# Kernel optimization log

Hardware: AMD Instinct MI355X
Metric: run time of the kernel (lower is better)

## Reference

```python
import jax, jax.numpy as jnp
from jax import lax
import numpy as np

B = 16384
EPS = 1e-5


def conv2d(x, w, b, pad):
    # x: [N,C,H,W], w: [O,I,kh,kw]
    y = lax.conv_general_dilated(x, w, (1, 1), [(pad, pad), (pad, pad)],
                                 dimension_numbers=("NCHW", "OIHW", "NCHW"))
    return y + b[None, :, None, None]


def maxpool2(x):
    return lax.reduce_window(x, -jnp.inf, lax.max, (1, 1, 2, 2), (1, 1, 2, 2), "VALID")


def setup_inputs() -> dict:
    key = jax.random.key(0)
    ks = jax.random.split(key, 16)
    n = jax.random.normal
    return {
        "x": n(ks[0], (B, 1, 28, 28), dtype=jnp.float32),
        "conv1_w": n(ks[1], (8, 1, 3, 3), dtype=jnp.float32) * 0.2,
        "conv1_b": n(ks[2], (8,), dtype=jnp.float32) * 0.1,
        "conv2_w": n(ks[3], (16, 8, 3, 3), dtype=jnp.float32) * 0.1,
        "conv2_b": n(ks[4], (16,), dtype=jnp.float32) * 0.1,
        "s1_w": n(ks[5], (4, 2), dtype=jnp.float32) * 0.5,
        "s1_b": n(ks[6], (4,), dtype=jnp.float32) * 0.1,
        "s2_w": n(ks[7], (2, 4), dtype=jnp.float32) * 0.5,
        "s2_b": n(ks[8], (2,), dtype=jnp.float32) * 0.1,
        "filt_w": n(ks[9], (1, 1, 2, 2), dtype=jnp.float32) * 0.5,
        "filt_b": n(ks[10], (1,), dtype=jnp.float32) * 0.1,
        "fc1_w": n(ks[11], (64, 787), dtype=jnp.float32) * 0.03,
        "fc1_b": n(ks[12], (64,), dtype=jnp.float32) * 0.1,
        "fc2_w": n(ks[13], (4, 64), dtype=jnp.float32) * 0.1,
        "fc2_b": n(ks[14], (4,), dtype=jnp.float32) * 0.1,
        "bn_g": jnp.ones((4,), dtype=jnp.float32),
        "bn_b": jnp.zeros((4,), dtype=jnp.float32),
    }


def reference(x, conv1_w, conv1_b, conv2_w, conv2_b, s1_w, s1_b, s2_w, s2_b,
              filt_w, filt_b, fc1_w, fc1_b, fc2_w, fc2_b, bn_g, bn_b):
    bsz = x.shape[0]
    # feature extractor: conv3x3 -> relu -> maxpool2 (x2)
    f = maxpool2(jax.nn.relu(conv2d(x, conv1_w, conv1_b, 1)))        # [B,8,14,14]
    f = maxpool2(jax.nn.relu(conv2d(f, conv2_w, conv2_b, 1)))        # [B,16,7,7]
    flat = f.reshape(bsz, -1)                                        # [B,784]
    # sampler on first two features
    h = jnp.tanh(flat[:, :2] @ s1_w.T + s1_b)
    sampler_out = jax.nn.softmax(h @ s2_w.T + s2_b, axis=-1)         # [B,2]
    # conv filter: 2x2 stride-1 conv + sigmoid, mean over all patches
    logits = conv2d(x, filt_w, filt_b, 0)                            # [B,1,27,27]
    conv_out = jnp.mean(jax.nn.sigmoid(logits), axis=(1, 2, 3))[:, None]  # [B,1]
    combined = jnp.concatenate([flat, sampler_out, conv_out], axis=1)  # [B,787]
    out = jax.nn.relu(combined @ fc1_w.T + fc1_b) @ fc2_w.T + fc2_b    # [B,4]
    # BatchNorm1d, training mode (batch stats, biased variance)
    mu = jnp.mean(out, axis=0)
    var = jnp.var(out, axis=0)
    return (out - mu) * lax.rsqrt(var + EPS) * bn_g + bn_b
```

## Files before the change

kernel.cpp:

```cpp
#include <hip/hip_runtime.h>
#include <hip/hip_fp16.h>
#include <math.h>

#define NBATCH 16384
#define EPSV 1e-5f
#define IMG 8

typedef short short8 __attribute__((ext_vector_type(8)));
typedef _Float16 half8_t __attribute__((ext_vector_type(8)));
typedef short short2v __attribute__((ext_vector_type(2)));
typedef float f32x4 __attribute__((ext_vector_type(4)));
union V8 { uint4 u; short8 s; };
union VH { uint4 u; half8_t h; };

__device__ __forceinline__ unsigned short f2bf(float f) {
    unsigned int x = __float_as_uint(f);
    return (unsigned short)((x + 0x7fffu + ((x >> 16) & 1u)) >> 16);
}
__device__ __forceinline__ __half2 u2h(unsigned int u) { return __builtin_bit_cast(__half2, u); }
__device__ __forceinline__ unsigned int h2u(__half2 h) { return __builtin_bit_cast(unsigned int, h); }

__global__ __launch_bounds__(256) void k_prep(
    const float* __restrict__ fc1w, const float* __restrict__ w2,
    const float* __restrict__ w1, const float* __restrict__ b1,
    unsigned short* __restrict__ wt, unsigned short* __restrict__ af16,
    unsigned int* __restrict__ w1h2, unsigned int* __restrict__ b1h2)
{
    int i = blockIdx.x * 256 + threadIdx.x;
    if (i < 51200) {
        int n = i / 800, k = i - n * 800;
        float v = (k < 787) ? fc1w[n * 787 + k] : 0.f;
        wt[i] = f2bf(v);
    } else if (i < 52736) {
        int a = i - 51200;
        int slot = a >> 7, rem = a & 127, oc = rem >> 3, ic = rem & 7;
        float v = (slot < 9) ? w2[oc * 72 + ic * 9 + slot] : 0.f;
        af16[a] = __half_as_ushort(__float2half(v));
    } else if (i < 52808) {
        int k = i - 52736;
        unsigned int hb = __half_as_ushort(__float2half(w1[k]));
        w1h2[k] = hb | (hb << 16);
    } else if (i < 52816) {
        int k = i - 52808;
        unsigned int hb = __half_as_ushort(__float2half(b1[k]));
        b1h2[k] = hb | (hb << 16);
    }
}

__global__ __launch_bounds__(256) void k_conv(
    const float* __restrict__ x,
    const float* __restrict__ s1w, const float* __restrict__ s1b,
    const float* __restrict__ s2w, const float* __restrict__ s2b,
    const float* __restrict__ fw, const float* __restrict__ fb,
    const float* __restrict__ b2,
    const unsigned short* __restrict__ Afg,
    const unsigned int* __restrict__ w1h2g,
    const unsigned int* __restrict__ b1h2g,
    unsigned short* __restrict__ comb)
{
    const int t = threadIdx.x;
    const int b_base = blockIdx.x * IMG;

    __shared__ unsigned int sxu[30 * 18];
    __shared__ __align__(16) unsigned short sf1[16 * 136];
    __shared__ __align__(16) float scomb[800];
    __shared__ float sred[4];
    __shared__ float ssm[27];
    __shared__ float sb2s[16];

    for (int i = t; i < 540; i += 256) sxu[i] = 0u;
    if (t < 60) {
        int R, C;
        if (t < 16)      { R = 0;      C = t; }
        else if (t < 32) { R = 15;     C = t - 16; }
        else if (t < 46) { R = t - 31; C = 0; }
        else             { R = t - 45; C = 15; }
        *reinterpret_cast<uint4*>(&sf1[R * 136 + C * 8]) = uint4{0u, 0u, 0u, 0u};
    }
    if (t >= 64 && t < 80) scomb[784 + (t - 64)] = 0.f;
    if (t >= 128 && t < 136) ssm[t - 128] = s1w[t - 128];
    else if (t >= 136 && t < 140) ssm[t - 128] = s1b[t - 136];
    else if (t >= 140 && t < 148) ssm[t - 128] = s2w[t - 140];
    else if (t >= 148 && t < 150) ssm[t - 128] = s2b[t - 148];
    else if (t >= 150 && t < 154) ssm[t - 128] = fw[t - 150];
    else if (t == 154) ssm[26] = fb[0];
    if (t >= 160 && t < 176) sb2s[t - 160] = b2[t - 160];
    __syncthreads();

    const __half2 fwh0 = __float2half2_rn(ssm[22]);
    const __half2 fwh1 = __float2half2_rn(ssm[23]);
    const __half2 fwh2 = __float2half2_rn(ssm[24]);
    const __half2 fwh3 = __float2half2_rn(ssm[25]);
    const __half2 fbh  = __float2half2_rn(ssm[26]);

    const int l = t & 63, w = t >> 6;
    const int n = l & 15, g = l >> 4;
    const int qr = n & 7;
    const int q = (qr < 7) ? qr : 6;
    const int dr = n >> 3;
    int offs[3];
    VH af[3];
    #pragma unroll
    for (int s = 0; s < 3; ++s) {
        const int slot = s * 4 + g;
        const int u = slot / 3, v = slot - 3 * (slot / 3);
        offs[s] = (slot <= 8) ? (u * 136 + v * 8) : 0;
        af[s].u = *reinterpret_cast<const uint4*>(Afg + ((slot * 16 + n) << 3));
    }

    for (int img = 0; img < IMG; ++img) {
        const int b = b_base + img;
        const float* xb = x + (size_t)b * 784;

        for (int u0 = t; u0 < 420; u0 += 256) {
            int r = u0 / 15, ww = u0 - r * 15;
            __half2 h2;
            if (ww == 0)       h2 = __floats2half2_rn(0.f, xb[r * 28]);
            else if (ww == 14) h2 = __floats2half2_rn(xb[r * 28 + 27], 0.f);
            else               h2 = __floats2half2_rn(xb[r * 28 + 2 * ww - 1],
                                                      xb[r * 28 + 2 * ww]);
            sxu[(r + 1) * 18 + ww] = h2u(h2);
        }
        __syncthreads();

        {
            float fsum = 0.f;
            #pragma unroll
            for (int it = 0; it < 2; ++it) {
                int u0 = t + it * 256;
                if (u0 < 378) {
                    int r = u0 / 14, cp = u0 - (u0 / 14) * 14;
                    unsigned int A1 = sxu[(r + 1) * 18 + cp], B1 = sxu[(r + 1) * 18 + cp + 1];
                    unsigned int A2 = sxu[(r + 2) * 18 + cp], B2 = sxu[(r + 2) * 18 + cp + 1];
                    __half2 al1 = u2h(__builtin_amdgcn_alignbit(B1, A1, 16));
                    __half2 al2 = u2h(__builtin_amdgcn_alignbit(B2, A2, 16));
                    __half2 acc = __hfma2(fwh0, al1,
                                  __hfma2(fwh1, u2h(B1),
                                  __hfma2(fwh2, al2,
                                  __hfma2(fwh3, u2h(B2), fbh))));
                    float2 f = __half22float2(acc);
                    fsum += __frcp_rn(1.f + __expf(-f.x));
                    if (cp < 13) fsum += __frcp_rn(1.f + __expf(-f.y));
                }
            }
            #pragma unroll
            for (int off = 32; off > 0; off >>= 1)
                fsum += __shfl_xor(fsum, off, 64);
            if ((t & 63) == 0) sred[t >> 6] = fsum;
        }

        if (t < 196) {
            const int p = t / 14, j = t - (t / 14) * 14;
            unsigned int A[4], B[4], M[4];
            #pragma unroll
            for (int u = 0; u < 4; ++u) {
                A[u] = sxu[(2 * p + u) * 18 + j];
                B[u] = sxu[(2 * p + u) * 18 + j + 1];
                M[u] = __builtin_amdgcn_alignbit(B[u], A[u], 16);
            }
            unsigned short outv[8];
            #pragma unroll
            for (int oc = 0; oc < 8; ++oc) {
                __half2 a0 = u2h(b1h2g[oc]), a1 = a0;
                #pragma unroll
                for (int u = 0; u < 3; ++u) {
                    #pragma unroll
                    for (int v = 0; v < 3; ++v) {
                        const __half2 wv = u2h(w1h2g[oc * 9 + u * 3 + v]);
                        const unsigned int p0 = (v == 0) ? A[u]     : ((v == 1) ? M[u]     : B[u]);
                        const unsigned int p1 = (v == 0) ? A[u + 1] : ((v == 1) ? M[u + 1] : B[u + 1]);
                        a0 = __hfma2(wv, u2h(p0), a0);
                        a1 = __hfma2(wv, u2h(p1), a1);
                    }
                }
                short2v s0 = __builtin_bit_cast(short2v, a0);
                short2v s1 = __builtin_bit_cast(short2v, a1);
                short2v mm = __builtin_elementwise_max(s0, s1);
                short m = mm[0] > mm[1] ? mm[0] : mm[1];
                if (m < 0) m = 0;
                outv[oc] = (unsigned short)m;
            }
            *reinterpret_cast<uint4*>(&sf1[(p + 1) * 136 + (j + 1) * 8]) =
                *reinterpret_cast<const uint4*>(outv);
        }
        __syncthreads();

        for (int pp = w; pp < 7; pp += 4) {
            const int rbase = (2 * pp + dr) * 136 + (2 * q) * 8;
            f32x4 acc0 = {0.f, 0.f, 0.f, 0.f}, acc1 = {0.f, 0.f, 0.f, 0.f};
            #pragma unroll
            for (int s = 0; s < 3; ++s) {
                VH b0, b1v;
                b0.u  = *reinterpret_cast<const uint4*>(&sf1[rbase + offs[s]]);
                b1v.u = *reinterpret_cast<const uint4*>(&sf1[rbase + 8 + offs[s]]);
                acc0 = __builtin_amdgcn_mfma_f32_16x16x32_f16(af[s].h, b0.h, acc0, 0, 0, 0);
                acc1 = __builtin_amdgcn_mfma_f32_16x16x32_f16(af[s].h, b1v.h, acc1, 0, 0, 0);
            }
            #pragma unroll
            for (int i = 0; i < 4; ++i) {
                const float bias = sb2s[4 * g + i];
                float m = fmaxf(acc0[i], acc1[i]);
                m = fmaxf(m, __shfl_xor(m, 8, 64));
                if (n < 7)
                    scomb[(4 * g + i) * 49 + pp * 7 + q] = fmaxf(m + bias, 0.f);
            }
        }
        __syncthreads();

        if (t == 0) {
            scomb[786] = (sred[0] + sred[1] + sred[2] + sred[3]) * (1.f / 729.f);
            float f0 = scomb[0], f1 = scomb[1];
            float h[4];
            #pragma unroll
            for (int k = 0; k < 4; ++k) {
                float y = fmaf(f0, ssm[k * 2], fmaf(f1, ssm[k * 2 + 1], ssm[8 + k]));
                float e = __expf(2.f * y);
                h[k] = (e - 1.f) * __frcp_rn(e + 1.f);
            }
            float l0 = ssm[20], l1 = ssm[21];
            #pragma unroll
            for (int k = 0; k < 4; ++k) {
                l0 = fmaf(h[k], ssm[12 + k], l0);
                l1 = fmaf(h[k], ssm[16 + k], l1);
            }
            float mx = fmaxf(l0, l1);
            float e0 = __expf(l0 - mx), e1 = __expf(l1 - mx);
            float inv = __frcp_rn(e0 + e1);
            scomb[784] = e0 * inv;
            scomb[785] = e1 * inv;
        }
        __syncthreads();

        if (t < 100) {
            const float4* sp = reinterpret_cast<const float4*>(scomb);
            float4 f0 = sp[2 * t], f1 = sp[2 * t + 1];
            uint4 o;
            o.x = (unsigned int)f2bf(f0.x) | ((unsigned int)f2bf(f0.y) << 16);
            o.y = (unsigned int)f2bf(f0.z) | ((unsigned int)f2bf(f0.w) << 16);
            o.z = (unsigned int)f2bf(f1.x) | ((unsigned int)f2bf(f1.y) << 16);
            o.w = (unsigned int)f2bf(f1.z) | ((unsigned int)f2bf(f1.w) << 16);
            reinterpret_cast<uint4*>(comb)[(size_t)b * 100 + t] = o;
        }
        __syncthreads();
    }
}

__global__ __launch_bounds__(256) void k_fc(
    const unsigned short* __restrict__ A,
    const unsigned short* __restrict__ Bw,
    const float* __restrict__ fc1b,
    const float* __restrict__ fc2w, const float* __restrict__ fc2b,
    float* __restrict__ out, float* __restrict__ part)
{
    __shared__ uint4 Asm[2][256];
    __shared__ uint4 Bsm[2][256];
    __shared__ float sh[64][68];
    __shared__ float sfc2[4][64];
    __shared__ float pacc[4][8];

    const int t = threadIdx.x;
    const int w = t >> 6, l = t & 63;
    const int blk = blockIdx.x;

    sfc2[t >> 6][t & 63] = fc2w[t];

    const int srow = t >> 2, skbp = t & 3;
    const int skbl = skbp ^ ((srow >> 1) & 3);
    const uint4* Ag = reinterpret_cast<const uint4*>(A) + ((size_t)blk * 64 + srow) * 100;
    const uint4* Bg = reinterpret_cast<const uint4*>(Bw) + (size_t)srow * 100;
    const int sidx = srow * 4 + skbp;

    const int arow = w * 16 + (l & 15);
    const int aidx = arow * 4 + ((l >> 4) ^ ((arow >> 1) & 3));
    int bidx[4];
    #pragma unroll
    for (int nf = 0; nf < 4; ++nf) {
        int nn = nf * 16 + (l & 15);
        bidx[nf] = nn * 4 + ((l >> 4) ^ ((nn >> 1) & 3));
    }

    f32x4 acc0 = {0.f, 0.f, 0.f, 0.f}, acc1 = acc0, acc2 = acc0, acc3 = acc0;

    Asm[0][sidx] = Ag[skbl];
    Bsm[0][sidx] = Bg[skbl];

    int buf = 0;
    for (int s = 0; s < 25; ++s) {
        __syncthreads();
        if (s < 24) {
            Asm[buf ^ 1][sidx] = Ag[(s + 1) * 4 + skbl];
            Bsm[buf ^ 1][sidx] = Bg[(s + 1) * 4 + skbl];
        }
        V8 av; av.u = Asm[buf][aidx];
        V8 b0; b0.u = Bsm[buf][bidx[0]];
        V8 b1; b1.u = Bsm[buf][bidx[1]];
        V8 b2; b2.u = Bsm[buf][bidx[2]];
        V8 b3; b3.u = Bsm[buf][bidx[3]];
        acc0 = __builtin_amdgcn_mfma_f32_16x16x32_bf16(av.s, b0.s, acc0, 0, 0, 0);
        acc1 = __builtin_amdgcn_mfma_f32_16x16x32_bf16(av.s, b1.s, acc1, 0, 0, 0);
        acc2 = __builtin_amdgcn_mfma_f32_16x16x32_bf16(av.s, b2.s, acc2, 0, 0, 0);
        acc3 = __builtin_amdgcn_mfma_f32_16x16x32_bf16(av.s, b3.s, acc3, 0, 0, 0);
        buf ^= 1;
    }

    {
        const int c0 = l & 15, r0 = w * 16 + (l >> 4) * 4;
        float fb0 = fc1b[c0], fb1 = fc1b[16 + c0], fb2 = fc1b[32 + c0], fb3 = fc1b[48 + c0];
        #pragma unroll
        for (int r = 0; r < 4; ++r) {
            sh[r0 + r][c0]      = fmaxf(acc0[r] + fb0, 0.f);
            sh[r0 + r][16 + c0] = fmaxf(acc1[r] + fb1, 0.f);
            sh[r0 + r][32 + c0] = fmaxf(acc2[r] + fb2, 0.f);
            sh[r0 + r][48 + c0] = fmaxf(acc3[r] + fb3, 0.f);
        }
    }
    __syncthreads();

    {
        const int row = t >> 2, oo = t & 3;
        float s = fc2b[oo];
        #pragma unroll 8
        for (int o = 0; o < 64; ++o)
            s = fmaf(sh[row][o], sfc2[oo][o], s);
        out[((size_t)blk * 64 + row) * 4 + oo] = s;

        float rs = s, rq = s * s;
        #pragma unroll
        for (int off = 4; off < 64; off <<= 1) {
            rs += __shfl_xor(rs, off, 64);
            rq += __shfl_xor(rq, off, 64);
        }
        if (l < 4) pacc[w][l] = rs;
        else if (l < 8) pacc[w][l] = rq;
    }
    __syncthreads();
    if (t < 8)
        part[blk * 8 + t] = pacc[0][t] + pacc[1][t] + pacc[2][t] + pacc[3][t];
}

__global__ void k_bnfinal(const float* __restrict__ part,
                          const float* __restrict__ g, const float* __restrict__ bb,
                          float* __restrict__ ss, int nblocks)
{
    const int t = threadIdx.x;
    float s[8];
    #pragma unroll
    for (int i = 0; i < 8; ++i) s[i] = 0.f;
    for (int idx = t; idx < nblocks; idx += 64)
        #pragma unroll
        for (int i = 0; i < 8; ++i) s[i] += part[idx * 8 + i];
    #pragma unroll
    for (int i = 0; i < 8; ++i)
        #pragma unroll
        for (int off = 32; off > 0; off >>= 1)
            s[i] += __shfl_xor(s[i], off, 64);
    if (t == 0) {
        const float invB = 1.f / 16384.f;
        #pragma unroll
        for (int j = 0; j < 4; ++j) {
            float mu = s[j] * invB;
            float var = s[4 + j] * invB - mu * mu;
            float sc = g[j] * rsqrtf(var + EPSV);
            ss[j] = sc;
            ss[4 + j] = bb[j] - mu * sc;
        }
    }
}

__global__ __launch_bounds__(256) void k_bnapply(const float* __restrict__ ss,
                                                 float* __restrict__ out)
{
    const int row = blockIdx.x * 256 + threadIdx.x;
    float4 v = reinterpret_cast<float4*>(out)[row];
    v.x = fmaf(v.x, ss[0], ss[4]);
    v.y = fmaf(v.y, ss[1], ss[5]);
    v.z = fmaf(v.z, ss[2], ss[6]);
    v.w = fmaf(v.w, ss[3], ss[7]);
    reinterpret_cast<float4*>(out)[row] = v;
}

__global__ __launch_bounds__(256) void k_transpose_fb(const float* __restrict__ in,
                                                      float* __restrict__ out)
{
    int i = blockIdx.x * 256 + threadIdx.x;
    if (i < 787 * 64) {
        int k = i >> 6, o = i & 63;
        out[i] = in[o * 787 + k];
    }
}

#define SF1F(ic, r, c) sf1[(ic) * 324 + (r) * 20 + (c)]

__global__ __launch_bounds__(256) void k_fused_fb(
    const float* __restrict__ x,
    const float* __restrict__ w1, const float* __restrict__ b1,
    const float* __restrict__ w2, const float* __restrict__ b2,
    const float* __restrict__ s1w, const float* __restrict__ s1b,
    const float* __restrict__ s2w, const float* __restrict__ s2b,
    const float* __restrict__ fw, const float* __restrict__ fb,
    const float* __restrict__ wt, const float* __restrict__ fc1b,
    const float* __restrict__ fc2w, const float* __restrict__ fc2b,
    float* __restrict__ pre)
{
    const int b = blockIdx.x;
    const int t = threadIdx.x;

    __shared__ float sxA[30][20];
    __shared__ float sxB[30][20];
    __shared__ float sf1[8 * 324];
    __shared__ float scomb[788];
    __shared__ float sw1[72];
    __shared__ float sb1[8];
    __shared__ float sw2p[16 * 76];
    __shared__ float sb2[16];
    __shared__ float sh1p[4][64];
    __shared__ float sh1[64];
    __shared__ float sred[4];
    __shared__ float ssm[27];

    for (int i = t; i < 600; i += 256) { (&sxA[0][0])[i] = 0.f; (&sxB[0][0])[i] = 0.f; }
    for (int i = t; i < 8 * 324; i += 256) sf1[i] = 0.f;
    if (t < 72) sw1[t] = w1[t];
    if (t < 8) sb1[t] = b1[t];
    for (int i = t; i < 1152; i += 256) {
        int oc = i / 72, rem = i - oc * 72;
        sw2p[oc * 76 + rem] = w2[i];
    }
    if (t < 16) sb2[t] = b2[t];
    if (t < 8) ssm[t] = s1w[t];
    else if (t < 12) ssm[t] = s1b[t - 8];
    else if (t < 20) ssm[t] = s2w[t - 12];
    else if (t < 22) ssm[t] = s2b[t - 20];
    else if (t < 26) ssm[t] = fw[t - 22];
    else if (t == 26) ssm[t] = fb[0];
    __syncthreads();

    const float* xb = x + (size_t)b * 784;
    for (int i = t; i < 784; i += 256) {
        int r = i / 28, c = i - (i / 28) * 28;
        float v = xb[i];
        int pr = r + 1, pc = c + 1;
        if (pc <= 15) sxA[pr][pc] = v;
        if (pc >= 14) sxB[pr][pc - 14] = v;
    }
    __syncthreads();

    {
        const float fw00 = ssm[22], fw01 = ssm[23], fw10 = ssm[24], fw11 = ssm[25];
        const float fbv = ssm[26];
        float fsum = 0.f;
        for (int i = t; i < 729; i += 256) {
            int r = i / 27, c = i - (i / 27) * 27;
            float x00, x01, x10, x11;
            if (c <= 13) {
                x00 = sxA[r + 1][c + 1]; x01 = sxA[r + 1][c + 2];
                x10 = sxA[r + 2][c + 1]; x11 = sxA[r + 2][c + 2];
            } else {
                int cb = c - 14;
                x00 = sxB[r + 1][cb + 1]; x01 = sxB[r + 1][cb + 2];
                x10 = sxB[r + 2][cb + 1]; x11 = sxB[r + 2][cb + 2];
            }
            float v = fbv;
            v = fmaf(x00, fw00, v); v = fmaf(x01, fw01, v);
            v = fmaf(x10, fw10, v); v = fmaf(x11, fw11, v);
            fsum += 1.f / (1.f + expf(-v));
        }
        #pragma unroll
        for (int off = 32; off > 0; off >>= 1)
            fsum += __shfl_xor(fsum, off, 64);
        if ((t & 63) == 0) sred[t >> 6] = fsum;
    }

    {
        const int half = t >> 7;
        const int id = t & 127;
        if (id < 112) {
            const int p = id >> 3, oc = id & 7;
            const float* base = half ? &sxB[0][0] : &sxA[0][0];
            float X[4][16];
            #pragma unroll
            for (int u = 0; u < 4; ++u) {
                const float4* rp = reinterpret_cast<const float4*>(base + (2 * p + u) * 20);
                float4 a = rp[0], bb4 = rp[1], c4 = rp[2], d4 = rp[3];
                X[u][0] = a.x;  X[u][1] = a.y;  X[u][2] = a.z;  X[u][3] = a.w;
                X[u][4] = bb4.x; X[u][5] = bb4.y; X[u][6] = bb4.z; X[u][7] = bb4.w;
                X[u][8] = c4.x;  X[u][9] = c4.y;  X[u][10] = c4.z; X[u][11] = c4.w;
                X[u][12] = d4.x; X[u][13] = d4.y; X[u][14] = d4.z; X[u][15] = d4.w;
            }
            float W[9];
            #pragma unroll
            for (int k = 0; k < 9; ++k) W[k] = sw1[oc * 9 + k];
            const float bias = sb1[oc];
            const int j0 = half * 7;
            #pragma unroll
            for (int jj = 0; jj < 7; ++jj) {
                float m = 0.f;
                #pragma unroll
                for (int dr = 0; dr < 2; ++dr)
                    #pragma unroll
                    for (int dc = 0; dc < 2; ++dc) {
                        float acc = bias;
                        #pragma unroll
                        for (int u = 0; u < 3; ++u)
                            #pragma unroll
                            for (int v = 0; v < 3; ++v)
                                acc = fmaf(X[dr + u][2 * jj + dc + v], W[u * 3 + v], acc);
                        m = fmaxf(m, acc);
                    }
                SF1F(oc, p + 1, j0 + jj + 1) = m;
            }
        }
    }
    __syncthreads();

    if (t < 112) {
        const int p = t >> 4, oc = t & 15;
        const float bias = sb2[oc];
        float acc[7][4];
        #pragma unroll
        for (int jj = 0; jj < 7; ++jj)
            #pragma unroll
            for (int s = 0; s < 4; ++s) acc[jj][s] = bias;
        for (int ic = 0; ic < 8; ++ic) {
            float X[4][16];
            #pragma unroll
            for (int u = 0; u < 4; ++u) {
                const float4* rp = reinterpret_cast<const float4*>(&SF1F(ic, 2 * p + u, 0));
                float4 a = rp[0], bb4 = rp[1], c4 = rp[2], d4 = rp[3];
                X[u][0] = a.x;  X[u][1] = a.y;  X[u][2] = a.z;  X[u][3] = a.w;
                X[u][4] = bb4.x; X[u][5] = bb4.y; X[u][6] = bb4.z; X[u][7] = bb4.w;
                X[u][8] = c4.x;  X[u][9] = c4.y;  X[u][10] = c4.z; X[u][11] = c4.w;
                X[u][12] = d4.x; X[u][13] = d4.y; X[u][14] = d4.z; X[u][15] = d4.w;
            }
            float W[9];
            #pragma unroll
            for (int k = 0; k < 9; ++k) W[k] = sw2p[oc * 76 + ic * 9 + k];
            #pragma unroll
            for (int jj = 0; jj < 7; ++jj)
                #pragma unroll
                for (int dr = 0; dr < 2; ++dr)
                    #pragma unroll
                    for (int dc = 0; dc < 2; ++dc)
                        #pragma unroll
                        for (int u = 0; u < 3; ++u)
                            #pragma unroll
                            for (int v = 0; v < 3; ++v)
                                acc[jj][dr * 2 + dc] =
                                    fmaf(X[dr + u][2 * jj + dc + v], W[u * 3 + v], acc[jj][dr * 2 + dc]);
        }
        #pragma unroll
        for (int jj = 0; jj < 7; ++jj) {
            float m = fmaxf(fmaxf(acc[jj][0], acc[jj][1]), fmaxf(acc[jj][2], acc[jj][3]));
            scomb[oc * 49 + p * 7 + jj] = fmaxf(m, 0.f);
        }
    }
    __syncthreads();

    if (t == 0) {
        scomb[786] = (sred[0] + sred[1] + sred[2] + sred[3]) * (1.f / 729.f);
        float f0 = scomb[0], f1 = scomb[1];
        float h[4];
        #pragma unroll
        for (int k = 0; k < 4; ++k)
            h[k] = tanhf(fmaf(f0, ssm[k * 2], fmaf(f1, ssm[k * 2 + 1], ssm[8 + k])));
        float l0 = ssm[20], l1 = ssm[21];
        #pragma unroll
        for (int k = 0; k < 4; ++k) {
            l0 = fmaf(h[k], ssm[12 + k], l0);
            l1 = fmaf(h[k], ssm[16 + k], l1);
        }
        float mx = fmaxf(l0, l1);
        float e0 = expf(l0 - mx), e1 = expf(l1 - mx);
        float inv = 1.f / (e0 + e1);
        scomb[784] = e0 * inv;
        scomb[785] = e1 * inv;
    }
    __syncthreads();

    {
        const int o = t & 63, w = t >> 6;
        const int k0 = w * 197;
        const int k1 = (w == 3) ? 787 : k0 + 197;
        const float* wp = wt + (size_t)k0 * 64 + o;
        float acc = 0.f;
        #pragma unroll 4
        for (int k = k0; k < k1; ++k) {
            acc = fmaf(scomb[k], *wp, acc);
            wp += 64;
        }
        sh1p[w][o] = acc;
    }
    __syncthreads();
    if (t < 64)
        sh1[t] = fmaxf(sh1p[0][t] + sh1p[1][t] + sh1p[2][t] + sh1p[3][t] + fc1b[t], 0.f);
    __syncthreads();

    {
        const int oo = t >> 6, lane = t & 63;
        float v = sh1[lane] * fc2w[oo * 64 + lane];
        #pragma unroll
        for (int off = 32; off > 0; off >>= 1)
            v += __shfl_xor(v, off, 64);
        if (lane == 0) pre[(size_t)b * 4 + oo] = v + fc2b[oo];
    }
}

__global__ __launch_bounds__(256) void k_bnstat_fb(const float* __restrict__ pre,
                                                   float* __restrict__ part)
{
    const int t = threadIdx.x;
    const int row = blockIdx.x * 256 + t;
    float4 v = reinterpret_cast<const float4*>(pre)[row];
    float s0 = v.x, s1 = v.y, s2 = v.z, s3 = v.w;
    float q0 = v.x * v.x, q1 = v.y * v.y, q2 = v.z * v.z, q3 = v.w * v.w;
    #pragma unroll
    for (int off = 32; off > 0; off >>= 1) {
        s0 += __shfl_xor(s0, off, 64);
        s1 += __shfl_xor(s1, off, 64);
        s2 += __shfl_xor(s2, off, 64);
        s3 += __shfl_xor(s3, off, 64);
        q0 += __shfl_xor(q0, off, 64);
        q1 += __shfl_xor(q1, off, 64);
        q2 += __shfl_xor(q2, off, 64);
        q3 += __shfl_xor(q3, off, 64);
    }
    __shared__ float acc[4][8];
    if ((t & 63) == 0) {
        int w = t >> 6;
        acc[w][0] = s0; acc[w][1] = s1; acc[w][2] = s2; acc[w][3] = s3;
        acc[w][4] = q0; acc[w][5] = q1; acc[w][6] = q2; acc[w][7] = q3;
    }
    __syncthreads();
    if (t < 8)
        part[blockIdx.x * 8 + t] = acc[0][t] + acc[1][t] + acc[2][t] + acc[3][t];
}

extern "C" void kernel_launch(void* const* d_in, const int* in_sizes, int n_in,
                              void* d_out, int out_size, void* d_ws, size_t ws_size,
                              hipStream_t stream)
{
    const float* x    = (const float*)d_in[0];
    const float* w1   = (const float*)d_in[1];
    const float* b1   = (const float*)d_in[2];
    const float* w2   = (const float*)d_in[3];
    const float* b2   = (const float*)d_in[4];
    const float* s1w  = (const float*)d_in[5];
    const float* s1b  = (const float*)d_in[6];
    const float* s2w  = (const float*)d_in[7];
    const float* s2b  = (const float*)d_in[8];
    const float* fw   = (const float*)d_in[9];
    const float* fb   = (const float*)d_in[10];
    const float* fc1w = (const float*)d_in[11];
    const float* fc1b = (const float*)d_in[12];
    const float* fc2w = (const float*)d_in[13];
    const float* fc2b = (const float*)d_in[14];
    const float* bng  = (const float*)d_in[15];
    const float* bnb  = (const float*)d_in[16];

    float* out = (float*)d_out;

    const size_t COMB_BYTES = (size_t)NBATCH * 800 * 2;
    const size_t WT_BYTES   = 64 * 800 * 2;
    const size_t AF16_BYTES = 1536 * 2;
    const size_t W1H2_BYTES = 72 * 4;
    const size_t B1H2_BYTES = 8 * 4;
    const size_t PART_BYTES = 256 * 8 * 4;
    const size_t NEED = COMB_BYTES + WT_BYTES + AF16_BYTES + W1H2_BYTES +
                        B1H2_BYTES + PART_BYTES + 32;

    if (ws_size >= NEED) {
        char* p = (char*)d_ws;
        unsigned short* comb = (unsigned short*)p;                     p += COMB_BYTES;
        unsigned short* wtbf = (unsigned short*)p;                     p += WT_BYTES;
        unsigned short* af16 = (unsigned short*)p;                     p += AF16_BYTES;
        unsigned int*   w1h2 = (unsigned int*)p;                       p += W1H2_BYTES;
        unsigned int*   b1h2 = (unsigned int*)p;                       p += B1H2_BYTES;
        float*          part = (float*)p;                              p += PART_BYTES;
        float*          ss   = (float*)p;

        k_prep<<<207, 256, 0, stream>>>(fc1w, w2, w1, b1, wtbf, af16, w1h2, b1h2);
        k_conv<<<NBATCH / IMG, 256, 0, stream>>>(x, s1w, s1b, s2w, s2b, fw, fb, b2,
                                                 af16, w1h2, b1h2, comb);
        k_fc<<<256, 256, 0, stream>>>(comb, wtbf, fc1b, fc2w, fc2b, out, part);
        k_bnfinal<<<1, 64, 0, stream>>>(part, bng, bnb, ss, 256);
        k_bnapply<<<64, 256, 0, stream>>>(ss, out);
    } else {
        float* part = (float*)d_ws;
        float* ss   = part + 512;
        float* wt   = ss + 8;

        k_transpose_fb<<<197, 256, 0, stream>>>(fc1w, wt);
        k_fused_fb<<<NBATCH, 256, 0, stream>>>(x, w1, b1, w2, b2, s1w, s1b, s2w, s2b,
                                               fw, fb, wt, fc1b, fc2w, fc2b, out);
        k_bnstat_fb<<<64, 256, 0, stream>>>(out, part);
        k_bnfinal<<<1, 64, 0, stream>>>(part, bng, bnb, ss, 64);
        k_bnapply<<<64, 256, 0, stream>>>(ss, out);
    }
}
```

Measured before the change: 106.6 us.

## Give each wavefront its own images in conv kernel to drop block barriers

The conv kernel now gives each of the four wavefronts its own private LDS buffers and its own set of four images. All per-image phases (input staging, sigmoid filter sum, conv1, conv2 MFMA, sampler, bf16 pack) run within a single wave with no __syncthreads. The sigmoid-sum reduction is now a plain wave shuffle with no shared partials. This removes block-wide barrier stalls and the partial thread utilisation of phases that used 196 or 100 of 256 threads. In exchange LDS use per block grows roughly fourfold, the grid is halved, and correctness relies on in-order LDS access within a wave without explicit fences.

Result: no change. 105.3 us (-1.3%).

```diff
diff --git a/kernel.cpp b/kernel.cpp
--- a/kernel.cpp
+++ b/kernel.cpp
@@ -4,7 +4,7 @@
 
 #define NBATCH 16384
 #define EPSV 1e-5f
-#define IMG 8
+#define IMGW 4
 
 typedef short short8 __attribute__((ext_vector_type(8)));
 typedef _Float16 half8_t __attribute__((ext_vector_type(8)));
@@ -59,33 +59,37 @@
     unsigned short* __restrict__ comb)
 {
     const int t = threadIdx.x;
-    const int b_base = blockIdx.x * IMG;
-
-    __shared__ unsigned int sxu[30 * 18];
-    __shared__ __align__(16) unsigned short sf1[16 * 136];
-    __shared__ __align__(16) float scomb[800];
-    __shared__ float sred[4];
+    const int w = t >> 6, l = t & 63;
+
+    __shared__ unsigned int sxu_all[4][30 * 18];
+    __shared__ __align__(16) unsigned short sf1_all[4][16 * 136];
+    __shared__ __align__(16) float scomb_all[4][800];
     __shared__ float ssm[27];
     __shared__ float sb2s[16];
 
-    for (int i = t; i < 540; i += 256) sxu[i] = 0u;
-    if (t < 60) {
+    unsigned int* sxu = sxu_all[w];
+    unsigned short* sf1 = sf1_all[w];
+    float* scomb = scomb_all[w];
+
+    if (t < 8) ssm[t] = s1w[t];
+    else if (t < 12) ssm[t] = s1b[t - 8];
+    else if (t < 20) ssm[t] = s2w[t - 12];
+    else if (t < 22) ssm[t] = s2b[t - 20];
+    else if (t < 26) ssm[t] = fw[t - 22];
+    else if (t == 26) ssm[26] = fb[0];
+    if (t >= 32 && t < 48) sb2s[t - 32] = b2[t - 32];
+    __syncthreads();
+
+    for (int i = l; i < 540; i += 64) sxu[i] = 0u;
+    if (l < 60) {
         int R, C;
-        if (t < 16)      { R = 0;      C = t; }
-        else if (t < 32) { R = 15;     C = t - 16; }
-        else if (t < 46) { R = t - 31; C = 0; }
-        else             { R = t - 45; C = 15; }
+        if (l < 16)      { R = 0;      C = l; }
+        else if (l < 32) { R = 15;     C = l - 16; }
+        else if (l < 46) { R = l - 31; C = 0; }
+        else             { R = l - 45; C = 15; }
         *reinterpret_cast<uint4*>(&sf1[R * 136 + C * 8]) = uint4{0u, 0u, 0u, 0u};
     }
-    if (t >= 64 && t < 80) scomb[784 + (t - 64)] = 0.f;
-    if (t >= 128 && t < 136) ssm[t - 128] = s1w[t - 128];
-    else if (t >= 136 && t < 140) ssm[t - 128] = s1b[t - 136];
-    else if (t >= 140 && t < 148) ssm[t - 128] = s2w[t - 140];
-    else if (t >= 148 && t < 150) ssm[t - 128] = s2b[t - 148];
-    else if (t >= 150 && t < 154) ssm[t - 128] = fw[t - 150];
-    else if (t == 154) ssm[26] = fb[0];
-    if (t >= 160 && t < 176) sb2s[t - 160] = b2[t - 160];
-    __syncthreads();
+    if (l < 16) scomb[784 + l] = 0.f;
 
     const __half2 fwh0 = __float2half2_rn(ssm[22]);
     const __half2 fwh1 = __float2half2_rn(ssm[23]);
@@ -93,7 +97,6 @@
     const __half2 fwh3 = __float2half2_rn(ssm[25]);
     const __half2 fbh  = __float2half2_rn(ssm[26]);
 
-    const int l = t & 63, w = t >> 6;
     const int n = l & 15, g = l >> 4;
     const int qr = n & 7;
     const int q = (qr < 7) ? qr : 6;
@@ -108,12 +111,13 @@
         af[s].u = *reinterpret_cast<const uint4*>(Afg + ((slot * 16 + n) << 3));
     }
 
-    for (int img = 0; img < IMG; ++img) {
-        const int b = b_base + img;
+    #pragma unroll 1
+    for (int img = 0; img < IMGW; ++img) {
+        const int b = (blockIdx.x * 4 + w) * IMGW + img;
         const float* xb = x + (size_t)b * 784;
 
-        for (int u0 = t; u0 < 420; u0 += 256) {
-            int r = u0 / 15, ww = u0 - r * 15;
+        for (int u0 = l; u0 < 420; u0 += 64) {
+            int r = u0 / 15, ww = u0 - (u0 / 15) * 15;
             __half2 h2;
             if (ww == 0)       h2 = __floats2half2_rn(0.f, xb[r * 28]);
             else if (ww == 14) h2 = __floats2half2_rn(xb[r * 28 + 27], 0.f);
@@ -121,36 +125,28 @@
                                                       xb[r * 28 + 2 * ww]);
             sxu[(r + 1) * 18 + ww] = h2u(h2);
         }
-        __syncthreads();
-
-        {
-            float fsum = 0.f;
-            #pragma unroll
-            for (int it = 0; it < 2; ++it) {
-                int u0 = t + it * 256;
-                if (u0 < 378) {
-                    int r = u0 / 14, cp = u0 - (u0 / 14) * 14;
-                    unsigned int A1 = sxu[(r + 1) * 18 + cp], B1 = sxu[(r + 1) * 18 + cp + 1];
-                    unsigned int A2 = sxu[(r + 2) * 18 + cp], B2 = sxu[(r + 2) * 18 + cp + 1];
-                    __half2 al1 = u2h(__builtin_amdgcn_alignbit(B1, A1, 16));
-                    __half2 al2 = u2h(__builtin_amdgcn_alignbit(B2, A2, 16));
-                    __half2 acc = __hfma2(fwh0, al1,
-                                  __hfma2(fwh1, u2h(B1),
-                                  __hfma2(fwh2, al2,
-                                  __hfma2(fwh3, u2h(B2), fbh))));
-                    float2 f = __half22float2(acc);
-                    fsum += __frcp_rn(1.f + __expf(-f.x));
-                    if (cp < 13) fsum += __frcp_rn(1.f + __expf(-f.y));
-                }
-            }
-            #pragma unroll
-            for (int off = 32; off > 0; off >>= 1)
-                fsum += __shfl_xor(fsum, off, 64);
-            if ((t & 63) == 0) sred[t >> 6] = fsum;
-        }
-
-        if (t < 196) {
-            const int p = t / 14, j = t - (t / 14) * 14;
+
+        float fsum = 0.f;
+        for (int u0 = l; u0 < 378; u0 += 64) {
+            int r = u0 / 14, cp = u0 - (u0 / 14) * 14;
+            unsigned int A1 = sxu[(r + 1) * 18 + cp], B1 = sxu[(r + 1) * 18 + cp + 1];
+            unsigned int A2 = sxu[(r + 2) * 18 + cp], B2 = sxu[(r + 2) * 18 + cp + 1];
+            __half2 al1 = u2h(__builtin_amdgcn_alignbit(B1, A1, 16));
+            __half2 al2 = u2h(__builtin_amdgcn_alignbit(B2, A2, 16));
+            __half2 acc = __hfma2(fwh0, al1,
+                          __hfma2(fwh1, u2h(B1),
+                          __hfma2(fwh2, al2,
+                          __hfma2(fwh3, u2h(B2), fbh))));
+            float2 f = __half22float2(acc);
+            fsum += __frcp_rn(1.f + __expf(-f.x));
+            if (cp < 13) fsum += __frcp_rn(1.f + __expf(-f.y));
+        }
+        #pragma unroll
+        for (int off = 32; off > 0; off >>= 1)
+            fsum += __shfl_xor(fsum, off, 64);
+
+        for (int i = l; i < 196; i += 64) {
+            const int p = i / 14, j = i - (i / 14) * 14;
             unsigned int A[4], B[4], M[4];
             #pragma unroll
             for (int u = 0; u < 4; ++u) {
@@ -183,9 +179,8 @@
             *reinterpret_cast<uint4*>(&sf1[(p + 1) * 136 + (j + 1) * 8]) =
                 *reinterpret_cast<const uint4*>(outv);
         }
-        __syncthreads();
-
-        for (int pp = w; pp < 7; pp += 4) {
+
+        for (int pp = 0; pp < 7; ++pp) {
             const int rbase = (2 * pp + dr) * 136 + (2 * q) * 8;
             f32x4 acc0 = {0.f, 0.f, 0.f, 0.f}, acc1 = {0.f, 0.f, 0.f, 0.f};
             #pragma unroll
@@ -205,10 +200,9 @@
                     scomb[(4 * g + i) * 49 + pp * 7 + q] = fmaxf(m + bias, 0.f);
             }
         }
-        __syncthreads();
-
-        if (t == 0) {
-            scomb[786] = (sred[0] + sred[1] + sred[2] + sred[3]) * (1.f / 729.f);
+
+        if (l == 0) {
+            scomb[786] = fsum * (1.f / 729.f);
             float f0 = scomb[0], f1 = scomb[1];
             float h[4];
             #pragma unroll
@@ -229,19 +223,17 @@
             scomb[784] = e0 * inv;
             scomb[785] = e1 * inv;
         }
-        __syncthreads();
-
-        if (t < 100) {
+
+        for (int u = l; u < 100; u += 64) {
             const float4* sp = reinterpret_cast<const float4*>(scomb);
-            float4 f0 = sp[2 * t], f1 = sp[2 * t + 1];
+            float4 f0 = sp[2 * u], f1 = sp[2 * u + 1];
             uint4 o;
             o.x = (unsigned int)f2bf(f0.x) | ((unsigned int)f2bf(f0.y) << 16);
             o.y = (unsigned int)f2bf(f0.z) | ((unsigned int)f2bf(f0.w) << 16);
             o.z = (unsigned int)f2bf(f1.x) | ((unsigned int)f2bf(f1.y) << 16);
             o.w = (unsigned int)f2bf(f1.z) | ((unsigned int)f2bf(f1.w) << 16);
-            reinterpret_cast<uint4*>(comb)[(size_t)b * 100 + t] = o;
-        }
-        __syncthreads();
+            reinterpret_cast<uint4*>(comb)[(size_t)b * 100 + u] = o;
+        }
     }
 }
 
@@ -679,8 +671,8 @@
         float*          ss   = (float*)p;
 
         k_prep<<<207, 256, 0, stream>>>(fc1w, w2, w1, b1, wtbf, af16, w1h2, b1h2);
-        k_conv<<<NBATCH / IMG, 256, 0, stream>>>(x, s1w, s1b, s2w, s2b, fw, fb, b2,
-                                                 af16, w1h2, b1h2, comb);
+        k_conv<<<NBATCH / (4 * IMGW), 256, 0, stream>>>(x, s1w, s1b, s2w, s2b, fw, fb, b2,
+                                                        af16, w1h2, b1h2, comb);
         k_fc<<<256, 256, 0, stream>>>(comb, wtbf, fc1b, fc2w, fc2b, out, part);
         k_bnfinal<<<1, 64, 0, stream>>>(part, bng, bnb, ss, 256);
         k_bnapply<<<64, 256, 0, stream>>>(ss, out);
```
